# Optimization experiments

Measured on AMD Instinct MI355X. Metric: run time of the kernel, lower is better.

Reference implementation:

```python
import jax, jax.numpy as jnp
import numpy as np
from jax import lax

H_IMG = 128; W_IMG = 128; C_IN = 200; NCLS = 16
N0 = H_IMG * W_IMG; N1 = 4096; N2 = 1024
K = 16  # neighbors(15) + 1 self loop, as in __init__
EPS = 1e-5
SLOPE = 0.01  # LeakyReLU default


def _leaky(x):
    return jnp.where(x >= 0, x, SLOPE * x)


def _bn1d(H, g, b):
    # BatchNorm1d in training mode: batch stats over node dim
    mu = H.mean(0)
    var = H.var(0)
    return (H - mu) * lax.rsqrt(var + EPS) * g + b


def _bn2d(x, g, b):
    mu = x.mean((0, 2, 3), keepdims=True)
    var = x.var((0, 2, 3), keepdims=True)
    return (x - mu) * lax.rsqrt(var + EPS) * g[None, :, None, None] + b[None, :, None, None]


def _ssconv(x, g, b, pw, pb, dw, db):
    # BN -> 1x1 pointwise conv -> LeakyReLU -> depthwise 5x5 conv -> LeakyReLU
    y = _bn2d(x, g, b)
    y = lax.conv_general_dilated(y, pw, (1, 1), 'SAME', dimension_numbers=('NCHW', 'OIHW', 'NCHW')) + pb[None, :, None, None]
    y = _leaky(y)
    c = dw.shape[0]
    y = lax.conv_general_dilated(y, dw, (1, 1), 'SAME', feature_group_count=c, dimension_numbers=('NCHW', 'OIHW', 'NCHW')) + db[None, :, None, None]
    return _leaky(y)


def _gcn(H, g, b, wt, bt, wo, bo, nbr):
    # GCNLayer_PyG, neighbors>0 branch. nbr: [N, K] neighbor indices (col), center broadcast (row)
    Hn = _bn1d(H, g, b)
    th = Hn @ wt + bt            # [N, 128]
    out = Hn @ wo + bo           # [N, F]
    A = jax.nn.sigmoid(jnp.einsum('nkd,nd->nk', th[nbr], th))  # sigmoid(<theta[col], theta[row]>)
    A = jax.nn.softmax(A, axis=1)                              # softmax over K neighbors
    agg = jnp.einsum('nk,nkf->nf', A, out[nbr])                # weighted neighbor aggregate
    return _leaky(agg), A


def _forward(x, hg, hb, hpw, hpb, hdw, hdb,
             e0_g, e0_b, e0_wt, e0_bt, e0_wo, e0_bo,
             e1_g, e1_b, e1_wt, e1_bt, e1_wo, e1_bo,
             d0_g, d0_b, d0_wt, d0_bt, d0_wo, d0_bo,
             tg, tb, tpw, tpb, tdw, tdb, ws, wb,
             S0, S1, Shat0, Shat1, nbr_a, nbr_b):
    x4 = x.transpose(2, 0, 1)[None]                 # [1, C, H, W]
    h0 = _ssconv(x4, hg, hb, hpw, hpb, hdw, hdb)    # [1, 128, H, W]
    H = h0[0].transpose(1, 2, 0).reshape(N0, -1)    # [N0, 128]
    enc0 = H
    H = Shat0 @ H                                   # pool to [N1, 128]
    H, A0 = _gcn(H, e0_g, e0_b, e0_wt, e0_bt, e0_wo, e0_bo, nbr_a)  # [N1, 64]
    enc1 = H
    H = Shat1 @ H                                   # pool to [N2, 64]
    H, A1 = _gcn(H, e1_g, e1_b, e1_wt, e1_bt, e1_wo, e1_bo, nbr_b)  # [N2, 32]
    # decoder
    H = S1 @ H                                      # unpool [N1, 32]
    H = jnp.concatenate([H, enc1], axis=-1)         # [N1, 96]
    H, Ad = _gcn(H, d0_g, d0_b, d0_wt, d0_bt, d0_wo, d0_bo, nbr_a)  # [N1, 64]
    H = S0 @ H                                      # unpool [N0, 64]
    H = jnp.concatenate([H, enc0], axis=-1)         # [N0, 192]
    t = H.reshape(1, H_IMG, W_IMG, -1).transpose(0, 3, 1, 2)
    f = _ssconv(t, tg, tb, tpw, tpb, tdw, tdb)      # [1, 128, H, W]
    f = f[0].transpose(1, 2, 0).reshape(N0, -1)
    Y = jax.nn.softmax(f @ ws + wb, axis=-1)        # [N0, NCLS]
    return Y


def setup_inputs() -> dict:
    key = jax.random.key(0)
    cnt = [0]
    def rn(shape, s=0.05):
        cnt[0] += 1
        return jax.random.normal(jax.random.fold_in(key, cnt[0]), shape, jnp.float32) * s
    x = rn((H_IMG, W_IMG, C_IN), 1.0)
    # balanced hierarchical assignment matrices (one-hot rows)
    S0 = jnp.zeros((N0, N1), jnp.float32).at[jnp.arange(N0), jnp.arange(N0) // (N0 // N1)].set(1.0)
    S1 = jnp.zeros((N1, N2), jnp.float32).at[jnp.arange(N1), jnp.arange(N1) // (N1 // N2)].set(1.0)
    Shat0 = (S0 / S0.sum(0, keepdims=True)).T
    Shat1 = (S1 / S1.sum(0, keepdims=True)).T
    # positions: pixel grid pooled through Shat (as in HiGCN.__init__)
    gx, gy = jnp.meshgrid(jnp.arange(H_IMG), jnp.arange(W_IMG), indexing='ij')
    pos = jnp.stack([gx, gy], -1).reshape(N0, 2).astype(jnp.float32)
    posA = Shat0 @ pos
    posB = Shat1 @ posA
    def knn(p):
        d = ((p[:, None, :] - p[None, :, :]) ** 2).sum(-1)
        return jnp.argsort(d, axis=1)[:, :K].astype(jnp.int32)  # self included (loop=True)
    nbr_a = knn(posA)  # [N1, K], used by enc0 and dec0
    nbr_b = knn(posB)  # [N2, K], used by enc1
    inp = dict(x=x, S0=S0, S1=S1, Shat0=Shat0, Shat1=Shat1, nbr_a=nbr_a, nbr_b=nbr_b)
    inp.update(hg=jnp.ones(C_IN), hb=jnp.zeros(C_IN), hpw=rn((128, C_IN, 1, 1)),
               hpb=jnp.zeros(128), hdw=rn((128, 1, 5, 5)), hdb=jnp.zeros(128))
    for tag, ci, co in (('e0', 128, 64), ('e1', 64, 32), ('d0', 96, 64)):
        inp[tag + '_g'] = jnp.ones(ci); inp[tag + '_b'] = jnp.zeros(ci)
        inp[tag + '_wt'] = rn((ci, 128)); inp[tag + '_bt'] = jnp.zeros(128)
        inp[tag + '_wo'] = rn((ci, co)); inp[tag + '_bo'] = jnp.zeros(co)
    inp.update(tg=jnp.ones(192), tb=jnp.zeros(192), tpw=rn((128, 192, 1, 1)),
               tpb=jnp.zeros(128), tdw=rn((128, 1, 5, 5)), tdb=jnp.zeros(128))
    inp.update(ws=rn((128, NCLS)), wb=jnp.zeros(NCLS))
    return inp


def reference(x, hg, hb, hpw, hpb, hdw, hdb,
              e0_g, e0_b, e0_wt, e0_bt, e0_wo, e0_bo,
              e1_g, e1_b, e1_wt, e1_bt, e1_wo, e1_bo,
              d0_g, d0_b, d0_wt, d0_bt, d0_wo, d0_bo,
              tg, tb, tpw, tpb, tdw, tdb, ws, wb,
              S0, S1, Shat0, Shat1, nbr_a, nbr_b):
    return _forward(x, hg, hb, hpw, hpb, hdw, hdb,
                    e0_g, e0_b, e0_wt, e0_bt, e0_wo, e0_bo,
                    e1_g, e1_b, e1_wt, e1_bt, e1_wo, e1_bo,
                    d0_g, d0_b, d0_wt, d0_bt, d0_wo, d0_bo,
                    tg, tb, tpw, tpb, tdw, tdb, ws, wb,
                    S0, S1, Shat0, Shat1, nbr_a, nbr_b)
```

## Files before the change

kernel.cpp:

```cpp
#include <hip/hip_runtime.h>
#include <hip/hip_bf16.h>
#include <math.h>

using bf16 = __hip_bfloat16;

#define H_IMG 128
#define W_IMG 128
#define C_IN  200
#define NCLS  16
#define N0    16384
#define N1    4096
#define N2    1024
#define KNB   16
#define EPS   1e-5f
#define SLOPE 0.01f

__device__ __forceinline__ float ldf(const float* p, long i) { return p[i]; }
__device__ __forceinline__ float ldf(const bf16* p, long i) { return __bfloat162float(p[i]); }
__device__ __forceinline__ float ldw(const void* p, long i, int fl) {
    return fl ? ((const float*)p)[i] : __bfloat162float(((const bf16*)p)[i]);
}
__device__ __forceinline__ float leaky(float v) { return v >= 0.f ? v : SLOPE * v; }

__device__ __forceinline__ float4 ld4(const float* p, long i) {
    return *reinterpret_cast<const float4*>(p + i);
}
__device__ __forceinline__ float4 ld4(const bf16* p, long i) {
    const ushort4 u = *reinterpret_cast<const ushort4*>(reinterpret_cast<const unsigned short*>(p) + i);
    float4 r;
    r.x = __uint_as_float((unsigned)u.x << 16);
    r.y = __uint_as_float((unsigned)u.y << 16);
    r.z = __uint_as_float((unsigned)u.z << 16);
    r.w = __uint_as_float((unsigned)u.w << 16);
    return r;
}

__device__ __forceinline__ int block_detect(const unsigned short* __restrict__ x) {
    __shared__ int cnt_s;
    if (threadIdx.x == 0) cnt_s = 0;
    __syncthreads();
    int cnt = 0;
    for (int i = threadIdx.x; i < 4096; i += blockDim.x) {
        unsigned short e = (unsigned short)((x[i] >> 7) & 0xFF);
        if (e >= 0xC0) cnt++;
    }
#pragma unroll
    for (int off = 32; off > 0; off >>= 1) cnt += __shfl_xor(cnt, off, 64);
    if ((threadIdx.x & 63) == 0) atomicAdd(&cnt_s, cnt);
    __syncthreads();
    return cnt_s > 32 ? 1 : 0;
}

__global__ __launch_bounds__(256) void bnx_kernel(const void* __restrict__ X, float2* __restrict__ part,
                                                  int* __restrict__ dflag) {
    int fl = block_detect((const unsigned short*)X);
    if (blockIdx.x == 0 && threadIdx.x == 0) *dflag = fl;
    int b = blockIdx.x, t = threadIdx.x;
    if (t >= C_IN) return;
    float s = 0.f, s2 = 0.f;
    if (fl) {
        const float* p = (const float*)X + (long)b * 64 * C_IN + t;
        for (int r = 0; r < 64; r++) { float v = p[(long)r * C_IN]; s += v; s2 += v * v; }
    } else {
        const bf16* p = (const bf16*)X + (long)b * 64 * C_IN + t;
        for (int r = 0; r < 64; r++) { float v = __bfloat162float(p[(long)r * C_IN]); s += v; s2 += v * v; }
    }
    part[(long)t * 256 + b] = make_float2(s, s2);
}

__device__ __forceinline__ void alphabeta_ld(const float2* __restrict__ partA, int npA, int splitC,
                                             const float2* __restrict__ partB, int npB,
                                             int Ci, float Pinv, const void* g, const void* b_,
                                             int fl, float* al, float* be) {
    int t = threadIdx.x;
    if (t < Ci) {
        const float2* src = (t < splitC) ? partA + (long)t * npA : partB + (long)(t - splitC) * npB;
        int np = (t < splitC) ? npA : npB;
        float s = 0.f, s2 = 0.f;
        const float4* p4 = (const float4*)src;
        for (int i = 0; i < (np >> 1); i++) { float4 v = p4[i]; s += v.x + v.z; s2 += v.y + v.w; }
        float mu = s * Pinv;
        float var = s2 * Pinv - mu * mu;
        float a = rsqrtf(var + EPS) * ldw(g, t, fl);
        al[t] = a;
        be[t] = ldw(b_, t, fl) - mu * a;
    }
    __syncthreads();
}

__device__ __forceinline__ void foldL(int j, const void* Wsrc, const void* bias,
                                      const float* al, const float* be,
                                      float* __restrict__ Wf, float* __restrict__ Bf,
                                      int Ci, int Co, int omajor, int fl, float* red) {
    int t = threadIdx.x;
    float acc = 0.f;
    for (int c = t; c < Ci; c += 256) {
        long idx = omajor ? (long)j * Ci + c : (long)c * Co + j;
        float w = ldw(Wsrc, idx, fl);
        Wf[(long)c * Co + j] = w * al[c];
        acc += w * be[c];
    }
    red[t] = acc; __syncthreads();
    for (int k = 128; k > 0; k >>= 1) { if (t < k) red[t] += red[t + k]; __syncthreads(); }
    if (t == 0) Bf[j] = ldw(bias, j, fl) + red[0];
}

__global__ __launch_bounds__(256) void bnfold_kernel(const float2* partA, int npA, int splitC,
                                                     const float2* partB, int npB, int P,
                                                     const void* g, const void* b_,
                                                     const void* Wt, const void* bias,
                                                     float* Wf, float* Bf, int Ci, int Co, int omajor,
                                                     const int* dflag) {
    __shared__ float al[256], be[256], red[256];
    int fl = *dflag;
    alphabeta_ld(partA, npA, splitC, partB, npB, Ci, 1.f / (float)P, g, b_, fl, al, be);
    foldL(blockIdx.x, Wt, bias, al, be, Wf, Bf, Ci, Co, omajor, fl, red);
}

__global__ __launch_bounds__(256) void bnfold2_kernel(const float2* partA, int npA, int splitC,
                                                      const float2* partB, int npB, int P,
                                                      const void* g, const void* b_,
                                                      const void* W1, const void* b1,
                                                      const void* W2, const void* b2,
                                                      float* Wf1, float* Bf1, float* Wf2, float* Bf2,
                                                      int Ci, int Co1, int Co2, const int* dflag) {
    __shared__ float al[256], be[256], red[256];
    int fl = *dflag;
    alphabeta_ld(partA, npA, splitC, partB, npB, Ci, 1.f / (float)P, g, b_, fl, al, be);
    int j = blockIdx.x;
    if (j < Co1) foldL(j, W1, b1, al, be, Wf1, Bf1, Ci, Co1, 0, fl, red);
    else         foldL(j - Co1, W2, b2, al, be, Wf2, Bf2, Ci, Co2, 0, fl, red);
}

template <typename T, int CI, int KT, int CAT>
__device__ __forceinline__ void gemmT_body(const T* __restrict__ In, const float* __restrict__ A2,
                                           const float* __restrict__ Wf, const float* __restrict__ Bf,
                                           float* __restrict__ Out) {
    __shared__ float wls[KT * 128];
    int t = threadIdx.x;
    int jq = t & 31, rp = t >> 5;
    int n0 = blockIdx.x * 16;
    int r0 = n0 + rp * 2, r1 = r0 + 1;
    float4 a0 = *reinterpret_cast<const float4*>(Bf + jq * 4);
    float4 a1 = a0;
    for (int kt = 0; kt < CI; kt += KT) {
        for (int e = t * 4; e < KT * 128; e += 1024)
            *reinterpret_cast<float4*>(&wls[e]) = *reinterpret_cast<const float4*>(&Wf[(long)kt * 128 + e]);
        __syncthreads();
        for (int cc = 0; cc < KT; cc += 4) {
            int c = kt + cc;
            float4 x0, x1;
            if (CAT) {
                if (c < 64) {
                    x0 = ld4(A2 + (long)(r0 >> 2) * 64, c);
                    x1 = ld4(A2 + (long)(r1 >> 2) * 64, c);
                } else {
                    x0 = ld4((const float*)In + (long)r0 * 128, c - 64);
                    x1 = ld4((const float*)In + (long)r1 * 128, c - 64);
                }
            } else {
                x0 = ld4(In + (long)r0 * CI, c);
                x1 = ld4(In + (long)r1 * CI, c);
            }
            const float* wp = &wls[cc * 128 + jq * 4];
            float4 w0 = *reinterpret_cast<const float4*>(wp);
            float4 w1 = *reinterpret_cast<const float4*>(wp + 128);
            float4 w2 = *reinterpret_cast<const float4*>(wp + 256);
            float4 w3 = *reinterpret_cast<const float4*>(wp + 384);
            a0.x += x0.x * w0.x; a0.y += x0.x * w0.y; a0.z += x0.x * w0.z; a0.w += x0.x * w0.w;
            a1.x += x1.x * w0.x; a1.y += x1.x * w0.y; a1.z += x1.x * w0.z; a1.w += x1.x * w0.w;
            a0.x += x0.y * w1.x; a0.y += x0.y * w1.y; a0.z += x0.y * w1.z; a0.w += x0.y * w1.w;
            a1.x += x1.y * w1.x; a1.y += x1.y * w1.y; a1.z += x1.y * w1.z; a1.w += x1.y * w1.w;
            a0.x += x0.z * w2.x; a0.y += x0.z * w2.y; a0.z += x0.z * w2.z; a0.w += x0.z * w2.w;
            a1.x += x1.z * w2.x; a1.y += x1.z * w2.y; a1.z += x1.z * w2.z; a1.w += x1.z * w2.w;
            a0.x += x0.w * w3.x; a0.y += x0.w * w3.y; a0.z += x0.w * w3.z; a0.w += x0.w * w3.w;
            a1.x += x1.w * w3.x; a1.y += x1.w * w3.y; a1.z += x1.w * w3.z; a1.w += x1.w * w3.w;
        }
        __syncthreads();
    }
    a0.x = leaky(a0.x); a0.y = leaky(a0.y); a0.z = leaky(a0.z); a0.w = leaky(a0.w);
    a1.x = leaky(a1.x); a1.y = leaky(a1.y); a1.z = leaky(a1.z); a1.w = leaky(a1.w);
    *reinterpret_cast<float4*>(Out + (long)r0 * 128 + jq * 4) = a0;
    *reinterpret_cast<float4*>(Out + (long)r1 * 128 + jq * 4) = a1;
}

__global__ __launch_bounds__(256) void gemmT_head_kernel(const void* In, const float* Wf, const float* Bf,
                                                         float* Out, const int* dflag) {
    if (*dflag) gemmT_body<float, C_IN, 40, 0>((const float*)In, nullptr, Wf, Bf, Out);
    else        gemmT_body<bf16,  C_IN, 40, 0>((const bf16*)In, nullptr, Wf, Bf, Out);
}

__global__ __launch_bounds__(256) void gemmT_tail_kernel(const float* InB, const float* InA,
                                                         const float* Wf, const float* Bf, float* Out) {
    gemmT_body<float, 192, 48, 1>(InB, InA, Wf, Bf, Out);
}

template <typename T, int ACT>
__device__ __forceinline__ void gemm4_body(const T* __restrict__ In, const float* __restrict__ Wf,
                                           const float* __restrict__ Bf, float* __restrict__ Out,
                                           int Ci, int Co, int blk) {
    int tid = blk * 256 + threadIdx.x;
    int Coq = Co >> 2;
    int n = tid / Coq;
    int j4 = (tid - n * Coq) << 2;
    const T* in = In + (long)n * Ci;
    const float* wp = Wf + j4;
    float4 acc = *reinterpret_cast<const float4*>(Bf + j4);
    for (int c = 0; c < Ci; c += 4) {
        float4 xv = ld4(in, c);
        float4 w0 = *reinterpret_cast<const float4*>(wp + (long)c * Co);
        float4 w1 = *reinterpret_cast<const float4*>(wp + (long)(c + 1) * Co);
        float4 w2 = *reinterpret_cast<const float4*>(wp + (long)(c + 2) * Co);
        float4 w3 = *reinterpret_cast<const float4*>(wp + (long)(c + 3) * Co);
        acc.x += xv.x * w0.x; acc.y += xv.x * w0.y; acc.z += xv.x * w0.z; acc.w += xv.x * w0.w;
        acc.x += xv.y * w1.x; acc.y += xv.y * w1.y; acc.z += xv.y * w1.z; acc.w += xv.y * w1.w;
        acc.x += xv.z * w2.x; acc.y += xv.z * w2.y; acc.z += xv.z * w2.z; acc.w += xv.z * w2.w;
        acc.x += xv.w * w3.x; acc.y += xv.w * w3.y; acc.z += xv.w * w3.z; acc.w += xv.w * w3.w;
    }
    if (ACT) { acc.x = leaky(acc.x); acc.y = leaky(acc.y); acc.z = leaky(acc.z); acc.w = leaky(acc.w); }
    *reinterpret_cast<float4*>(Out + (long)n * Co + j4) = acc;
}

template <int ACT, int SPLIT>
__device__ __forceinline__ void gemm4cat_body(const float* __restrict__ InA, int sA,
                                              const float* __restrict__ InB, int sB,
                                              const float* __restrict__ Wf, const float* __restrict__ Bf,
                                              float* __restrict__ Out, int Ci, int Co, int blk) {
    int tid = blk * 256 + threadIdx.x;
    int Coq = Co >> 2;
    int n = tid / Coq;
    int j4 = (tid - n * Coq) << 2;
    const float* ia = InA + (long)(n >> 2) * sA;
    const float* ib = InB + (long)n * sB;
    const float* wp = Wf + j4;
    float4 acc = *reinterpret_cast<const float4*>(Bf + j4);
    for (int c = 0; c < Ci; c += 4) {
        float4 xv = (c < SPLIT) ? *reinterpret_cast<const float4*>(ia + c)
                                : *reinterpret_cast<const float4*>(ib + (c - SPLIT));
        float4 w0 = *reinterpret_cast<const float4*>(wp + (long)c * Co);
        float4 w1 = *reinterpret_cast<const float4*>(wp + (long)(c + 1) * Co);
        float4 w2 = *reinterpret_cast<const float4*>(wp + (long)(c + 2) * Co);
        float4 w3 = *reinterpret_cast<const float4*>(wp + (long)(c + 3) * Co);
        acc.x += xv.x * w0.x; acc.y += xv.x * w0.y; acc.z += xv.x * w0.z; acc.w += xv.x * w0.w;
        acc.x += xv.y * w1.x; acc.y += xv.y * w1.y; acc.z += xv.y * w1.z; acc.w += xv.y * w1.w;
        acc.x += xv.z * w2.x; acc.y += xv.z * w2.y; acc.z += xv.z * w2.z; acc.w += xv.z * w2.w;
        acc.x += xv.w * w3.x; acc.y += xv.w * w3.y; acc.z += xv.w * w3.z; acc.w += xv.w * w3.w;
    }
    if (ACT) { acc.x = leaky(acc.x); acc.y = leaky(acc.y); acc.z = leaky(acc.z); acc.w = leaky(acc.w); }
    *reinterpret_cast<float4*>(Out + (long)n * Co + j4) = acc;
}

__global__ __launch_bounds__(256) void gemm2_f32_kernel(const float* In,
                                                        const float* W1, const float* B1, float* O1, int Co1,
                                                        const float* W2, const float* B2, float* O2, int Co2,
                                                        int Ci, int nb1) {
    int b = blockIdx.x;
    if (b < nb1) gemm4_body<float, 0>(In, W1, B1, O1, Ci, Co1, b);
    else         gemm4_body<float, 0>(In, W2, B2, O2, Ci, Co2, b - nb1);
}

template <int SPLIT>
__global__ __launch_bounds__(256) void gemm2cat_kernel(const float* InA, int sA, const float* InB, int sB,
                                                       const float* W1, const float* B1, float* O1, int Co1,
                                                       const float* W2, const float* B2, float* O2, int Co2,
                                                       int Ci, int nb1) {
    int b = blockIdx.x;
    if (b < nb1) gemm4cat_body<0, SPLIT>(InA, sA, InB, sB, W1, B1, O1, Ci, Co1, b);
    else         gemm4cat_body<0, SPLIT>(InA, sA, InB, sB, W2, B2, O2, Ci, Co2, b - nb1);
}

__device__ __forceinline__ void dw_load(const void* dwp, const void* dbp, float* wl, float* bl, int fl) {
    int t = threadIdx.x;
    for (int e = t; e < 25 * 128; e += 256) {
        int o = e / 25, i = e - o * 25;
        wl[i * 128 + o] = ldw(dwp, e, fl);
    }
    if (t < 128) bl[t] = ldw(dbp, t, fl);
}

__device__ __forceinline__ float4 dw_compute(int p, int o0, const float* __restrict__ In,
                                             const float* wl, const float* bl) {
    int h = p >> 7, w = p & 127;
    float4 acc = *reinterpret_cast<const float4*>(&bl[o0]);
#pragma unroll
    for (int dh = -2; dh <= 2; dh++) {
        int hh = h + dh;
        if ((unsigned)hh >= (unsigned)H_IMG) continue;
#pragma unroll
        for (int dv = -2; dv <= 2; dv++) {
            int ww = w + dv;
            if ((unsigned)ww >= (unsigned)W_IMG) continue;
            float4 iv = *reinterpret_cast<const float4*>(&In[(long)(((hh << 7) + ww) << 7) + o0]);
            float4 wv = *reinterpret_cast<const float4*>(&wl[((dh + 2) * 5 + (dv + 2)) * 128 + o0]);
            acc.x += iv.x * wv.x; acc.y += iv.y * wv.y; acc.z += iv.z * wv.z; acc.w += iv.w * wv.w;
        }
    }
    acc.x = leaky(acc.x); acc.y = leaky(acc.y); acc.z = leaky(acc.z); acc.w = leaky(acc.w);
    return acc;
}

__global__ __launch_bounds__(256) void dwpool_kernel(const float* __restrict__ In, const void* dwp, const void* dbp,
                                                     float* __restrict__ R1out, float* __restrict__ H1b,
                                                     float2* __restrict__ pE0, float2* __restrict__ pTb,
                                                     const int* dflag) {
    __shared__ float wl[25 * 128];
    __shared__ float bl[128];
    __shared__ float sm[8 * 132];
    int fl = *dflag;
    dw_load(dwp, dbp, wl, bl, fl);
    __syncthreads();
    int t = threadIdx.x;
    int o0 = (t & 31) << 2, pxl = t >> 5;
    float s = 0.f, s2 = 0.f, rs = 0.f, rs2 = 0.f;
    for (int it = 0; it < 4; it++) {
        int p = blockIdx.x * 32 + it * 8 + pxl;
        float4 acc = dw_compute(p, o0, In, wl, bl);
        *reinterpret_cast<float4*>(&R1out[(long)p * 128 + o0]) = acc;
        *reinterpret_cast<float4*>(&sm[pxl * 132 + o0]) = acc;
        __syncthreads();
        if (t < 128) {
#pragma unroll
            for (int g = 0; g < 2; g++) {
                float v0 = sm[(g * 4 + 0) * 132 + t], v1 = sm[(g * 4 + 1) * 132 + t];
                float v2 = sm[(g * 4 + 2) * 132 + t], v3 = sm[(g * 4 + 3) * 132 + t];
                float h = 0.25f * (v0 + v1 + v2 + v3);
                H1b[(long)(blockIdx.x * 8 + it * 2 + g) * 128 + t] = h;
                s += h; s2 += h * h;
                rs += v0 + v1 + v2 + v3;
                rs2 += v0 * v0 + v1 * v1 + v2 * v2 + v3 * v3;
            }
        }
        __syncthreads();
    }
    if (t < 128) {
        pE0[(long)t * 512 + blockIdx.x] = make_float2(s, s2);
        pTb[(long)t * 512 + blockIdx.x] = make_float2(rs, rs2);
    }
}

__global__ __launch_bounds__(256) void dwcls_kernel(const float* __restrict__ In, const void* dwp, const void* dbp,
                                                    const void* wsw, const void* wb, void* __restrict__ out,
                                                    const int* dflag) {
    __shared__ float wl[25 * 128];
    __shared__ float bl[128];
    __shared__ float cw[2048];
    __shared__ float F[8 * 132];
    int fl = *dflag;
    dw_load(dwp, dbp, wl, bl, fl);
    int t = threadIdx.x;
    for (int e = t; e < 2048; e += 256) cw[e] = ldw(wsw, e, fl);
    __syncthreads();
    int o0 = (t & 31) << 2, pxl = t >> 5;
    int p = blockIdx.x * 8 + pxl;
    float4 acc = dw_compute(p, o0, In, wl, bl);
    *reinterpret_cast<float4*>(&F[pxl * 132 + o0]) = acc;
    __syncthreads();
    if (t < 128) {
        int px = t >> 4, j = t & 15;
        float a = ldw(wb, j, fl);
        const float* fp = &F[px * 132];
#pragma unroll 8
        for (int c = 0; c < 128; c += 4) {
            float4 fv = *reinterpret_cast<const float4*>(fp + c);
            a += fv.x * cw[c * 16 + j] + fv.y * cw[(c + 1) * 16 + j]
               + fv.z * cw[(c + 2) * 16 + j] + fv.w * cw[(c + 3) * 16 + j];
        }
        float m = a;
#pragma unroll
        for (int s = 8; s > 0; s >>= 1) m = fmaxf(m, __shfl_xor(m, s, 16));
        float e = expf(a - m);
        float d = e;
#pragma unroll
        for (int s = 8; s > 0; s >>= 1) d += __shfl_xor(d, s, 16);
        float r = e / d;
        long oi = (long)(blockIdx.x * 8 + px) * 16 + j;
        if (fl) ((float*)out)[oi] = r;
        else ((bf16*)out)[oi] = __float2bfloat16(r);
    }
}

template <int MODE>
__global__ __launch_bounds__(256) void attn_fused_kernel(const float* __restrict__ th, const float* __restrict__ outm,
                                                         const int* __restrict__ nbr, float* __restrict__ dst, int co,
                                                         float* __restrict__ H2b,
                                                         float2* __restrict__ partP, float2* __restrict__ partS,
                                                         int snp) {
    int wid = threadIdx.x >> 6, l = threadIdx.x & 63;
    int n = blockIdx.x * 4 + wid;
    float r0 = th[(long)n * 128 + l];
    float r1 = th[(long)n * 128 + 64 + l];
    int mk[KNB];
    float av[KNB];
#pragma unroll
    for (int k = 0; k < KNB; k++) {
        int m = nbr[n * KNB + k];
        mk[k] = m;
        float v = r0 * th[(long)m * 128 + l] + r1 * th[(long)m * 128 + 64 + l];
#pragma unroll
        for (int off = 32; off > 0; off >>= 1) v += __shfl_xor(v, off, 64);
        av[k] = 1.f / (1.f + expf(-v));
    }
    float amax = av[0];
#pragma unroll
    for (int k = 1; k < KNB; k++) amax = fmaxf(amax, av[k]);
    float den = 0.f;
#pragma unroll
    for (int k = 0; k < KNB; k++) { av[k] = expf(av[k] - amax); den += av[k]; }
    float rden = 1.f / den;
    float val = 0.f;
    if (l < co) {
        float acc = 0.f;
#pragma unroll
        for (int k = 0; k < KNB; k++) acc += av[k] * outm[(long)mk[k] * co + l];
        val = leaky(acc * rden);
        dst[(long)n * co + l] = val;
    }
    __shared__ float sm[4][64];
    sm[wid][l] = (l < co) ? val : 0.f;
    __syncthreads();
    if (wid == 0 && l < co) {
        float a = sm[0][l], bb = sm[1][l], c = sm[2][l], d = sm[3][l];
        float su = a + bb + c + d;
        float sq = a * a + bb * bb + c * c + d * d;
        if (MODE == 0) {
            float h = 0.25f * su;
            H2b[(long)blockIdx.x * 64 + l] = h;
            partP[(long)l * snp + blockIdx.x] = make_float2(h, h * h);
            partS[(long)l * snp + blockIdx.x] = make_float2(su, sq);
        } else {
            partS[(long)l * snp + blockIdx.x] = make_float2(4.f * su, 4.f * sq);
        }
    }
}

extern "C" void kernel_launch(void* const* d_in, const int* in_sizes, int n_in,
                              void* d_out, int out_size, void* d_ws, size_t ws_size,
                              hipStream_t stream) {
    bool dict = (in_sizes[1] > 1000000);
    int I_x, I_nbr_a, I_nbr_b, I_hg, I_ws, I_e0, I_e1, I_d0, I_tg;
    if (dict) {
        I_x = 0; I_nbr_a = 5; I_nbr_b = 6; I_hg = 7; I_e0 = 13; I_e1 = 19; I_d0 = 25; I_tg = 31; I_ws = 37;
    } else {
        I_x = 0; I_hg = 1; I_e0 = 7; I_e1 = 13; I_d0 = 19; I_tg = 25; I_ws = 31; I_nbr_a = 37; I_nbr_b = 38;
    }
    const void* x    = d_in[I_x];
    const int* nbr_a = (const int*)d_in[I_nbr_a];
    const int* nbr_b = (const int*)d_in[I_nbr_b];
    const void* hg   = d_in[I_hg + 0];
    const void* hb   = d_in[I_hg + 1];
    const void* hpw  = d_in[I_hg + 2];
    const void* hpb  = d_in[I_hg + 3];
    const void* hdw  = d_in[I_hg + 4];
    const void* hdb  = d_in[I_hg + 5];
    const void* e0_g = d_in[I_e0 + 0];
    const void* e0_b = d_in[I_e0 + 1];
    const void* e0_wt= d_in[I_e0 + 2];
    const void* e0_bt= d_in[I_e0 + 3];
    const void* e0_wo= d_in[I_e0 + 4];
    const void* e0_bo= d_in[I_e0 + 5];
    const void* e1_g = d_in[I_e1 + 0];
    const void* e1_b = d_in[I_e1 + 1];
    const void* e1_wt= d_in[I_e1 + 2];
    const void* e1_bt= d_in[I_e1 + 3];
    const void* e1_wo= d_in[I_e1 + 4];
    const void* e1_bo= d_in[I_e1 + 5];
    const void* d0_g = d_in[I_d0 + 0];
    const void* d0_b = d_in[I_d0 + 1];
    const void* d0_wt= d_in[I_d0 + 2];
    const void* d0_bt= d_in[I_d0 + 3];
    const void* d0_wo= d_in[I_d0 + 4];
    const void* d0_bo= d_in[I_d0 + 5];
    const void* tg   = d_in[I_tg + 0];
    const void* tb   = d_in[I_tg + 1];
    const void* tpw  = d_in[I_tg + 2];
    const void* tpb  = d_in[I_tg + 3];
    const void* tdw  = d_in[I_tg + 4];
    const void* tdb  = d_in[I_tg + 5];
    const void* wsw  = d_in[I_ws + 0];
    const void* wb   = d_in[I_ws + 1];

    float* W = (float*)d_ws;
    float*  WF1    = W + 0;
    float*  BF1    = W + 25600;
    float*  WF2    = W + 25728;
    float*  BF2    = W + 33920;
    int*    dflag  = (int*)(W + 33984);
    float2* P_HEAD = (float2*)(W + 34048);
    float2* P_E0   = (float2*)(W + 136448);
    float2* P_Tb   = (float2*)(W + 267520);
    float2* P_E1   = (float2*)(W + 398592);
    float2* P_D0a  = (float2*)(W + 529664);
    float2* P_D0b  = (float2*)(W + 546048);
    float2* P_Ta   = (float2*)(W + 677120);
    float*  R0     = W + 808192;
    float*  R1     = R0 + (long)N0 * 128;
    float*  T1     = R1 + (long)N0 * 128;
    float*  H1b    = T1 + (long)N0 * 128;
    float*  THb    = H1b + (long)N1 * 128;
    float*  OUTb   = THb + (long)N1 * 128;
    float*  ENC1   = OUTb + (long)N1 * 64;
    float*  H2b    = ENC1 + (long)N1 * 64;
    float*  HDb    = H2b + (long)N2 * 64;
    float*  HDEC   = HDb + (long)N2 * 32;

    bnx_kernel<<<256, 256, 0, stream>>>(x, P_HEAD, dflag);
    bnfold_kernel<<<128, 256, 0, stream>>>(P_HEAD, 256, C_IN, P_HEAD, 256, N0,
                                           hg, hb, hpw, hpb, WF1, BF1, C_IN, 128, 1, dflag);
    gemmT_head_kernel<<<1024, 256, 0, stream>>>(x, WF1, BF1, R0, dflag);
    dwpool_kernel<<<512, 256, 0, stream>>>(R0, hdw, hdb, R1, H1b, P_E0, P_Tb, dflag);
    bnfold2_kernel<<<192, 256, 0, stream>>>(P_E0, 512, 128, P_E0, 512, N1, e0_g, e0_b,
                                            e0_wt, e0_bt, e0_wo, e0_bo,
                                            WF1, BF1, WF2, BF2, 128, 128, 64, dflag);
    gemm2_f32_kernel<<<768, 256, 0, stream>>>(H1b, WF1, BF1, THb, 128, WF2, BF2, OUTb, 64, 128, 512);
    attn_fused_kernel<0><<<1024, 256, 0, stream>>>(THb, OUTb, nbr_a, ENC1, 64, H2b, P_E1, P_D0b, 1024);
    bnfold2_kernel<<<160, 256, 0, stream>>>(P_E1, 1024, 64, P_E1, 1024, N2, e1_g, e1_b,
                                            e1_wt, e1_bt, e1_wo, e1_bo,
                                            WF1, BF1, WF2, BF2, 64, 128, 32, dflag);
    gemm2_f32_kernel<<<160, 256, 0, stream>>>(H2b, WF1, BF1, THb, 128, WF2, BF2, OUTb, 32, 64, 128);
    attn_fused_kernel<1><<<256, 256, 0, stream>>>(THb, OUTb, nbr_b, HDb, 32, nullptr, nullptr, P_D0a, 256);
    bnfold2_kernel<<<192, 256, 0, stream>>>(P_D0a, 256, 32, P_D0b, 1024, N1, d0_g, d0_b,
                                            d0_wt, d0_bt, d0_wo, d0_bo,
                                            WF1, BF1, WF2, BF2, 96, 128, 64, dflag);
    gemm2cat_kernel<32><<<768, 256, 0, stream>>>(HDb, 32, ENC1, 64,
                                                 WF1, BF1, THb, 128, WF2, BF2, OUTb, 64, 96, 512);
    attn_fused_kernel<2><<<1024, 256, 0, stream>>>(THb, OUTb, nbr_a, HDEC, 64, nullptr, nullptr, P_Ta, 1024);
    bnfold_kernel<<<128, 256, 0, stream>>>(P_Ta, 1024, 64, P_Tb, 512, N0,
                                           tg, tb, tpw, tpb, WF1, BF1, 192, 128, 1, dflag);
    gemmT_tail_kernel<<<1024, 256, 0, stream>>>(R1, HDEC, WF1, BF1, T1);
    dwcls_kernel<<<2048, 256, 0, stream>>>(T1, tdw, tdb, wsw, wb, d_out, dflag);
}
```

Baseline: 949.2 us.

## Fuse BN weight folding into producer kernels via last-block completion counter

```diff
diff --git a/kernel.cpp b/kernel.cpp
--- a/kernel.cpp
+++ b/kernel.cpp
@@ -15,13 +15,10 @@
 #define EPS   1e-5f
 #define SLOPE 0.01f
 
-__device__ __forceinline__ float ldf(const float* p, long i) { return p[i]; }
-__device__ __forceinline__ float ldf(const bf16* p, long i) { return __bfloat162float(p[i]); }
+__device__ __forceinline__ float leaky(float v) { return v >= 0.f ? v : SLOPE * v; }
 __device__ __forceinline__ float ldw(const void* p, long i, int fl) {
     return fl ? ((const float*)p)[i] : __bfloat162float(((const bf16*)p)[i]);
 }
-__device__ __forceinline__ float leaky(float v) { return v >= 0.f ? v : SLOPE * v; }
-
 __device__ __forceinline__ float4 ld4(const float* p, long i) {
     return *reinterpret_cast<const float4*>(p + i);
 }
@@ -51,85 +48,109 @@
     return cnt_s > 32 ? 1 : 0;
 }
 
-__global__ __launch_bounds__(256) void bnx_kernel(const void* __restrict__ X, float2* __restrict__ part,
-                                                  int* __restrict__ dflag) {
-    int fl = block_detect((const unsigned short*)X);
-    if (blockIdx.x == 0 && threadIdx.x == 0) *dflag = fl;
-    int b = blockIdx.x, t = threadIdx.x;
-    if (t >= C_IN) return;
-    float s = 0.f, s2 = 0.f;
-    if (fl) {
-        const float* p = (const float*)X + (long)b * 64 * C_IN + t;
-        for (int r = 0; r < 64; r++) { float v = p[(long)r * C_IN]; s += v; s2 += v * v; }
-    } else {
-        const bf16* p = (const bf16*)X + (long)b * 64 * C_IN + t;
-        for (int r = 0; r < 64; r++) { float v = __bfloat162float(p[(long)r * C_IN]); s += v; s2 += v * v; }
-    }
-    part[(long)t * 256 + b] = make_float2(s, s2);
-}
-
-__device__ __forceinline__ void alphabeta_ld(const float2* __restrict__ partA, int npA, int splitC,
-                                             const float2* __restrict__ partB, int npB,
-                                             int Ci, float Pinv, const void* g, const void* b_,
-                                             int fl, float* al, float* be) {
+__device__ void fold_layer(const float2* __restrict__ pA, int npA, int splitC,
+                           const float2* __restrict__ pB, int npB,
+                           int CI, float Pinv, const void* g, const void* bt, int fl,
+                           const void* W1, const void* b1, int Co1, int w1f32,
+                           const void* W2, const void* b2, int Co2,
+                           float* __restrict__ WF1, float* __restrict__ BF1,
+                           float* __restrict__ WF2, float* __restrict__ BF2,
+                           float* al, float* be) {
     int t = threadIdx.x;
-    if (t < Ci) {
-        const float2* src = (t < splitC) ? partA + (long)t * npA : partB + (long)(t - splitC) * npB;
+    if (t < CI) {
+        const float2* src = (t < splitC) ? pA + (long)t * npA : pB + (long)(t - splitC) * npB;
         int np = (t < splitC) ? npA : npB;
         float s = 0.f, s2 = 0.f;
         const float4* p4 = (const float4*)src;
         for (int i = 0; i < (np >> 1); i++) { float4 v = p4[i]; s += v.x + v.z; s2 += v.y + v.w; }
         float mu = s * Pinv;
         float var = s2 * Pinv - mu * mu;
-        float a = rsqrtf(var + EPS) * ldw(g, t, fl);
-        al[t] = a;
-        be[t] = ldw(b_, t, fl) - mu * a;
-    }
-    __syncthreads();
-}
-
-__device__ __forceinline__ void foldL(int j, const void* Wsrc, const void* bias,
-                                      const float* al, const float* be,
-                                      float* __restrict__ Wf, float* __restrict__ Bf,
-                                      int Ci, int Co, int omajor, int fl, float* red) {
-    int t = threadIdx.x;
-    float acc = 0.f;
-    for (int c = t; c < Ci; c += 256) {
-        long idx = omajor ? (long)j * Ci + c : (long)c * Co + j;
-        float w = ldw(Wsrc, idx, fl);
-        Wf[(long)c * Co + j] = w * al[c];
-        acc += w * be[c];
-    }
-    red[t] = acc; __syncthreads();
-    for (int k = 128; k > 0; k >>= 1) { if (t < k) red[t] += red[t + k]; __syncthreads(); }
-    if (t == 0) Bf[j] = ldw(bias, j, fl) + red[0];
-}
-
-__global__ __launch_bounds__(256) void bnfold_kernel(const float2* partA, int npA, int splitC,
-                                                     const float2* partB, int npB, int P,
-                                                     const void* g, const void* b_,
-                                                     const void* Wt, const void* bias,
-                                                     float* Wf, float* Bf, int Ci, int Co, int omajor,
-                                                     const int* dflag) {
-    __shared__ float al[256], be[256], red[256];
-    int fl = *dflag;
-    alphabeta_ld(partA, npA, splitC, partB, npB, Ci, 1.f / (float)P, g, b_, fl, al, be);
-    foldL(blockIdx.x, Wt, bias, al, be, Wf, Bf, Ci, Co, omajor, fl, red);
-}
-
-__global__ __launch_bounds__(256) void bnfold2_kernel(const float2* partA, int npA, int splitC,
-                                                      const float2* partB, int npB, int P,
-                                                      const void* g, const void* b_,
-                                                      const void* W1, const void* b1,
-                                                      const void* W2, const void* b2,
-                                                      float* Wf1, float* Bf1, float* Wf2, float* Bf2,
-                                                      int Ci, int Co1, int Co2, const int* dflag) {
-    __shared__ float al[256], be[256], red[256];
-    int fl = *dflag;
-    alphabeta_ld(partA, npA, splitC, partB, npB, Ci, 1.f / (float)P, g, b_, fl, al, be);
-    int j = blockIdx.x;
-    if (j < Co1) foldL(j, W1, b1, al, be, Wf1, Bf1, Ci, Co1, 0, fl, red);
-    else         foldL(j - Co1, W2, b2, al, be, Wf2, Bf2, Ci, Co2, 0, fl, red);
+        float aa = rsqrtf(var + EPS) * ldw(g, t, fl);
+        al[t] = aa;
+        be[t] = ldw(bt, t, fl) - mu * aa;
+    }
+    __syncthreads();
+    for (int e = t; e < CI * Co1; e += 256) {
+        int c = e / Co1;
+        float w = w1f32 ? ((const float*)W1)[e] : ldw(W1, e, fl);
+        WF1[e] = w * al[c];
+    }
+    if (t < Co1) {
+        float s = ldw(b1, t, fl);
+        for (int c = 0; c < CI; c++) {
+            float w = w1f32 ? ((const float*)W1)[(long)c * Co1 + t] : ldw(W1, (long)c * Co1 + t, fl);
+            s += w * be[c];
+        }
+        BF1[t] = s;
+    }
+    if (W2) {
+        for (int e = t; e < CI * Co2; e += 256) {
+            int c = e / Co2;
+            WF2[e] = ldw(W2, e, fl) * al[c];
+        }
+        if (t < Co2) {
+            float s = ldw(b2, t, fl);
+            for (int c = 0; c < CI; c++) s += ldw(W2, (long)c * Co2 + t, fl) * be[c];
+            BF2[t] = s;
+        }
+    }
+}
+
+__device__ __forceinline__ bool last_block(int* cnt, int nblk, int* lds_flag) {
+    __syncthreads();
+    if (threadIdx.x == 0) {
+        __threadfence();
+        *lds_flag = (atomicAdd(cnt, 1) == nblk - 1);
+    }
+    __syncthreads();
+    if (!*lds_flag) return false;
+    __threadfence();
+    return true;
+}
+
+__global__ __launch_bounds__(256) void prep_kernel(const void* __restrict__ x,
+                                                   const void* __restrict__ hpw, const void* __restrict__ tpw,
+                                                   float* __restrict__ WHc, float* __restrict__ WTc,
+                                                   int* __restrict__ dflag, int* __restrict__ cnts) {
+    int fl = block_detect((const unsigned short*)x);
+    if (blockIdx.x == 0 && threadIdx.x == 0) *dflag = fl;
+    if (blockIdx.x == 0 && threadIdx.x < 8) cnts[threadIdx.x] = 0;
+    if (blockIdx.x < 8) {
+        for (long e = blockIdx.x * 256 + threadIdx.x; e < 128L * C_IN; e += 8 * 256) {
+            int j = (int)(e / C_IN), c = (int)(e - (long)j * C_IN);
+            WHc[(long)c * 128 + j] = ldw(hpw, e, fl);
+        }
+    } else {
+        for (long e = (blockIdx.x - 8) * 256 + threadIdx.x; e < 128L * 192; e += 8 * 256) {
+            int j = (int)(e / 192), c = (int)(e - (long)j * 192);
+            WTc[(long)c * 128 + j] = ldw(tpw, e, fl);
+        }
+    }
+}
+
+__global__ __launch_bounds__(256) void bnx_kernel(const void* __restrict__ X, float2* __restrict__ part,
+                                                  const float* __restrict__ WHc, const void* hpb,
+                                                  const void* hg, const void* hb_,
+                                                  float* __restrict__ WFh, float* __restrict__ BFh,
+                                                  int* cnt) {
+    int fl = block_detect((const unsigned short*)X);
+    int b = blockIdx.x, t = threadIdx.x;
+    if (t < C_IN) {
+        float s = 0.f, s2 = 0.f;
+        if (fl) {
+            const float* p = (const float*)X + (long)b * 64 * C_IN + t;
+            for (int r = 0; r < 64; r++) { float v = p[(long)r * C_IN]; s += v; s2 += v * v; }
+        } else {
+            const bf16* p = (const bf16*)X + (long)b * 64 * C_IN + t;
+            for (int r = 0; r < 64; r++) { float v = __bfloat162float(p[(long)r * C_IN]); s += v; s2 += v * v; }
+        }
+        part[(long)t * 256 + b] = make_float2(s, s2);
+    }
+    __shared__ int lastf;
+    if (!last_block(cnt, 256, &lastf)) return;
+    __shared__ float al[256], be[256];
+    fold_layer(part, 256, C_IN, part, 256, C_IN, 1.f / (float)N0, hg, hb_, fl,
+               WHc, hpb, 128, 1, nullptr, nullptr, 0, WFh, BFh, nullptr, nullptr, al, be);
 }
 
 template <typename T, int CI, int KT, int CAT>
@@ -155,8 +176,8 @@
                     x0 = ld4(A2 + (long)(r0 >> 2) * 64, c);
                     x1 = ld4(A2 + (long)(r1 >> 2) * 64, c);
                 } else {
-                    x0 = ld4((const float*)In + (long)r0 * 128, c - 64);
-                    x1 = ld4((const float*)In + (long)r1 * 128, c - 64);
+                    x0 = ld4((const float*)(const void*)In + (long)r0 * 128, c - 64);
+                    x1 = ld4((const float*)(const void*)In + (long)r1 * 128, c - 64);
                 }
             } else {
                 x0 = ld4(In + (long)r0 * CI, c);
@@ -302,7 +323,12 @@
 __global__ __launch_bounds__(256) void dwpool_kernel(const float* __restrict__ In, const void* dwp, const void* dbp,
                                                      float* __restrict__ R1out, float* __restrict__ H1b,
                                                      float2* __restrict__ pE0, float2* __restrict__ pTb,
-                                                     const int* dflag) {
+                                                     const int* dflag,
+                                                     const void* e0_wt, const void* e0_bt,
+                                                     const void* e0_wo, const void* e0_bo,
+                                                     const void* e0_g, const void* e0_b,
+                                                     float* WF1, float* BF1, float* WF2, float* BF2,
+                                                     int* cnt) {
     __shared__ float wl[25 * 128];
     __shared__ float bl[128];
     __shared__ float sm[8 * 132];
@@ -336,6 +362,11 @@
         pE0[(long)t * 512 + blockIdx.x] = make_float2(s, s2);
         pTb[(long)t * 512 + blockIdx.x] = make_float2(rs, rs2);
     }
+    __shared__ int lastf;
+    if (!last_block(cnt, 512, &lastf)) return;
+    __shared__ float al[256], be[256];
+    fold_layer(pE0, 512, 128, pE0, 512, 128, 1.f / (float)N1, e0_g, e0_b, fl,
+               e0_wt, e0_bt, 128, 0, e0_wo, e0_bo, 64, WF1, BF1, WF2, BF2, al, be);
 }
 
 __global__ __launch_bounds__(256) void dwcls_kernel(const float* __restrict__ In, const void* dwp, const void* dbp,
@@ -380,11 +411,16 @@
 }
 
 template <int MODE>
-__global__ __launch_bounds__(256) void attn_fused_kernel(const float* __restrict__ th, const float* __restrict__ outm,
-                                                         const int* __restrict__ nbr, float* __restrict__ dst, int co,
-                                                         float* __restrict__ H2b,
-                                                         float2* __restrict__ partP, float2* __restrict__ partS,
-                                                         int snp) {
+__global__ __launch_bounds__(256) void attn_fused_kernel(
+        const float* __restrict__ th, const float* __restrict__ outm,
+        const int* __restrict__ nbr, float* __restrict__ dst, int co,
+        float* __restrict__ H2b, float2* __restrict__ partP, float2* __restrict__ partS, int snp,
+        int* cnt, int nblk, const int* dflag,
+        const float2* fpA, int fnpA, int fsplit, const float2* fpB, int fnpB,
+        int fCI, float fPinv, const void* fg, const void* fb,
+        const void* fW1, const void* fb1, int fCo1, int fw1f32,
+        const void* fW2, const void* fb2, int fCo2,
+        float* fWF1, float* fBF1, float* fWF2, float* fBF2) {
     int wid = threadIdx.x >> 6, l = threadIdx.x & 63;
     int n = blockIdx.x * 4 + wid;
     float r0 = th[(long)n * 128 + l];
@@ -431,6 +467,12 @@
             partS[(long)l * snp + blockIdx.x] = make_float2(4.f * su, 4.f * sq);
         }
     }
+    __shared__ int lastf;
+    if (!last_block(cnt, nblk, &lastf)) return;
+    __shared__ float al[256], be[256];
+    int fl = *dflag;
+    fold_layer(fpA, fnpA, fsplit, fpB, fnpB, fCI, fPinv, fg, fb, fl,
+               fW1, fb1, fCo1, fw1f32, fW2, fb2, fCo2, fWF1, fBF1, fWF2, fBF2, al, be);
 }
 
 extern "C" void kernel_launch(void* const* d_in, const int* in_sizes, int n_in,
@@ -480,52 +522,66 @@
     const void* wb   = d_in[I_ws + 1];
 
     float* W = (float*)d_ws;
-    float*  WF1    = W + 0;
-    float*  BF1    = W + 25600;
-    float*  WF2    = W + 25728;
-    float*  BF2    = W + 33920;
-    int*    dflag  = (int*)(W + 33984);
-    float2* P_HEAD = (float2*)(W + 34048);
-    float2* P_E0   = (float2*)(W + 136448);
-    float2* P_Tb   = (float2*)(W + 267520);
-    float2* P_E1   = (float2*)(W + 398592);
-    float2* P_D0a  = (float2*)(W + 529664);
-    float2* P_D0b  = (float2*)(W + 546048);
-    float2* P_Ta   = (float2*)(W + 677120);
-    float*  R0     = W + 808192;
-    float*  R1     = R0 + (long)N0 * 128;
-    float*  T1     = R1 + (long)N0 * 128;
-    float*  H1b    = T1 + (long)N0 * 128;
-    float*  THb    = H1b + (long)N1 * 128;
-    float*  OUTb   = THb + (long)N1 * 128;
-    float*  ENC1   = OUTb + (long)N1 * 64;
-    float*  H2b    = ENC1 + (long)N1 * 64;
-    float*  HDb    = H2b + (long)N2 * 64;
-    float*  HDEC   = HDb + (long)N2 * 32;
-
-    bnx_kernel<<<256, 256, 0, stream>>>(x, P_HEAD, dflag);
-    bnfold_kernel<<<128, 256, 0, stream>>>(P_HEAD, 256, C_IN, P_HEAD, 256, N0,
-                                           hg, hb, hpw, hpb, WF1, BF1, C_IN, 128, 1, dflag);
-    gemmT_head_kernel<<<1024, 256, 0, stream>>>(x, WF1, BF1, R0, dflag);
-    dwpool_kernel<<<512, 256, 0, stream>>>(R0, hdw, hdb, R1, H1b, P_E0, P_Tb, dflag);
-    bnfold2_kernel<<<192, 256, 0, stream>>>(P_E0, 512, 128, P_E0, 512, N1, e0_g, e0_b,
-                                            e0_wt, e0_bt, e0_wo, e0_bo,
-                                            WF1, BF1, WF2, BF2, 128, 128, 64, dflag);
-    gemm2_f32_kernel<<<768, 256, 0, stream>>>(H1b, WF1, BF1, THb, 128, WF2, BF2, OUTb, 64, 128, 512);
-    attn_fused_kernel<0><<<1024, 256, 0, stream>>>(THb, OUTb, nbr_a, ENC1, 64, H2b, P_E1, P_D0b, 1024);
-    bnfold2_kernel<<<160, 256, 0, stream>>>(P_E1, 1024, 64, P_E1, 1024, N2, e1_g, e1_b,
-                                            e1_wt, e1_bt, e1_wo, e1_bo,
-                                            WF1, BF1, WF2, BF2, 64, 128, 32, dflag);
-    gemm2_f32_kernel<<<160, 256, 0, stream>>>(H2b, WF1, BF1, THb, 128, WF2, BF2, OUTb, 32, 64, 128);
-    attn_fused_kernel<1><<<256, 256, 0, stream>>>(THb, OUTb, nbr_b, HDb, 32, nullptr, nullptr, P_D0a, 256);
-    bnfold2_kernel<<<192, 256, 0, stream>>>(P_D0a, 256, 32, P_D0b, 1024, N1, d0_g, d0_b,
-                                            d0_wt, d0_bt, d0_wo, d0_bo,
-                                            WF1, BF1, WF2, BF2, 96, 128, 64, dflag);
+    float*  WHc   = W + 0;
+    float*  WTc   = W + 25600;
+    int*    dflag = (int*)(W + 50176);
+    int*    cnts  = (int*)(W + 50240);
+    float*  WFh   = W + 50304;
+    float*  BFh   = W + 75904;
+    float*  WF1e0 = W + 76032;
+    float*  BF1e0 = W + 92416;
+    float*  WF2e0 = W + 92544;
+    float*  BF2e0 = W + 100736;
+    float*  WF1e1 = W + 100800;
+    float*  BF1e1 = W + 108992;
+    float*  WF2e1 = W + 109120;
+    float*  BF2e1 = W + 111168;
+    float*  WF1d0 = W + 111200;
+    float*  BF1d0 = W + 123488;
+    float*  WF2d0 = W + 123616;
+    float*  BF2d0 = W + 129760;
+    float*  WFt   = W + 129824;
+    float*  BFt   = W + 154400;
+    float2* P_HEAD = (float2*)(W + 154528);
+    float2* P_E0   = (float2*)(W + 256928);
+    float2* P_Tb   = (float2*)(W + 388000);
+    float2* P_E1   = (float2*)(W + 519072);
+    float2* P_D0a  = (float2*)(W + 650144);
+    float2* P_D0b  = (float2*)(W + 666528);
+    float2* P_Ta   = (float2*)(W + 797600);
+    float*  R0    = W + 928672;
+    float*  R1    = R0 + (long)N0 * 128;
+    float*  T1    = R1 + (long)N0 * 128;
+    float*  H1b   = T1 + (long)N0 * 128;
+    float*  THb   = H1b + (long)N1 * 128;
+    float*  OUTb  = THb + (long)N1 * 128;
+    float*  ENC1  = OUTb + (long)N1 * 64;
+    float*  H2b   = ENC1 + (long)N1 * 64;
+    float*  HDb   = H2b + (long)N2 * 64;
+    float*  HDEC  = HDb + (long)N2 * 32;
+
+    prep_kernel<<<16, 256, 0, stream>>>(x, hpw, tpw, WHc, WTc, dflag, cnts);
+    bnx_kernel<<<256, 256, 0, stream>>>(x, P_HEAD, WHc, hpb, hg, hb, WFh, BFh, &cnts[0]);
+    gemmT_head_kernel<<<1024, 256, 0, stream>>>(x, WFh, BFh, R0, dflag);
+    dwpool_kernel<<<512, 256, 0, stream>>>(R0, hdw, hdb, R1, H1b, P_E0, P_Tb, dflag,
+                                           e0_wt, e0_bt, e0_wo, e0_bo, e0_g, e0_b,
+                                           WF1e0, BF1e0, WF2e0, BF2e0, &cnts[1]);
+    gemm2_f32_kernel<<<768, 256, 0, stream>>>(H1b, WF1e0, BF1e0, THb, 128,
+                                              WF2e0, BF2e0, OUTb, 64, 128, 512);
+    attn_fused_kernel<0><<<1024, 256, 0, stream>>>(THb, OUTb, nbr_a, ENC1, 64, H2b, P_E1, P_D0b, 1024,
+        &cnts[2], 1024, dflag, P_E1, 1024, 64, P_E1, 1024, 64, 1.f / (float)N2, e1_g, e1_b,
+        e1_wt, e1_bt, 128, 0, e1_wo, e1_bo, 32, WF1e1, BF1e1, WF2e1, BF2e1);
+    gemm2_f32_kernel<<<160, 256, 0, stream>>>(H2b, WF1e1, BF1e1, THb, 128,
+                                              WF2e1, BF2e1, OUTb, 32, 64, 128);
+    attn_fused_kernel<1><<<256, 256, 0, stream>>>(THb, OUTb, nbr_b, HDb, 32, nullptr, nullptr, P_D0a, 256,
+        &cnts[3], 256, dflag, P_D0a, 256, 32, P_D0b, 1024, 96, 1.f / (float)N1, d0_g, d0_b,
+        d0_wt, d0_bt, 128, 0, d0_wo, d0_bo, 64, WF1d0, BF1d0, WF2d0, BF2d0);
     gemm2cat_kernel<32><<<768, 256, 0, stream>>>(HDb, 32, ENC1, 64,
-                                                 WF1, BF1, THb, 128, WF2, BF2, OUTb, 64, 96, 512);
-    attn_fused_kernel<2><<<1024, 256, 0, stream>>>(THb, OUTb, nbr_a, HDEC, 64, nullptr, nullptr, P_Ta, 1024);
-    bnfold_kernel<<<128, 256, 0, stream>>>(P_Ta, 1024, 64, P_Tb, 512, N0,
-                                           tg, tb, tpw, tpb, WF1, BF1, 192, 128, 1, dflag);
-    gemmT_tail_kernel<<<1024, 256, 0, stream>>>(R1, HDEC, WF1, BF1, T1);
+                                                 WF1d0, BF1d0, THb, 128,
+                                                 WF2d0, BF2d0, OUTb, 64, 96, 512);
+    attn_fused_kernel<2><<<1024, 256, 0, stream>>>(THb, OUTb, nbr_a, HDEC, 64, nullptr, nullptr, P_Ta, 1024,
+        &cnts[4], 1024, dflag, P_Ta, 1024, 64, P_Tb, 512, 192, 1.f / (float)N0, tg, tb,
+        WTc, tpb, 128, 1, nullptr, nullptr, 0, WFt, BFt, nullptr, nullptr);
+    gemmT_tail_kernel<<<1024, 256, 0, stream>>>(R1, HDEC, WFt, BFt, T1);
     dwcls_kernel<<<2048, 256, 0, stream>>>(T1, tdw, tdb, wsw, wb, d_out, dflag);
 }
```

Result: slower. 1.209 ms (+27.4%).
